# Performance work log

Hardware: AMD Instinct MI355X
Metric: run time of the kernel (lower is better)

## Reference

```python
import jax, jax.numpy as jnp
import numpy as np

N, E = 50000, 800000
NFEAT, NHID, NCLASS = 128, 64, 40
LN_EPS = 1e-5


def setup_inputs() -> dict:
    key = jax.random.key(0)
    ks = jax.random.split(key, 10)
    x = jax.random.normal(ks[0], (N, NFEAT), dtype=jnp.float32)
    edge_index = jax.random.randint(ks[1], (2, E), 0, N, dtype=jnp.int32)
    adj_vals = jax.random.uniform(ks[2], (E,), dtype=jnp.float32)
    s1 = 1.0 / NHID ** 0.5
    W1 = jax.random.uniform(ks[3], (NFEAT, NHID), minval=-s1, maxval=s1, dtype=jnp.float32)
    s2 = 1.0 / (2 * NHID) ** 0.5
    a1 = jax.random.uniform(ks[4], (2 * NHID, 1), minval=-s2, maxval=s2, dtype=jnp.float32)
    s3 = 1.0 / NCLASS ** 0.5
    W2 = jax.random.uniform(ks[5], (NHID, NCLASS), minval=-s3, maxval=s3, dtype=jnp.float32)
    # residual projection Linear(nfeat, nclass)
    sl = 1.0 / NFEAT ** 0.5
    res_w = jax.random.uniform(ks[6], (NCLASS, NFEAT), minval=-sl, maxval=sl, dtype=jnp.float32)
    res_b = jax.random.uniform(ks[7], (NCLASS,), minval=-sl, maxval=sl, dtype=jnp.float32)
    ln_g = jnp.ones((NCLASS,), dtype=jnp.float32)
    ln_b = jnp.zeros((NCLASS,), dtype=jnp.float32)
    return {"x": x, "edge_index": edge_index, "adj_vals": adj_vals,
            "W1": W1, "a1": a1, "W2": W2, "res_w": res_w, "res_b": res_b,
            "ln_g": ln_g, "ln_b": ln_b}


def reference(x, edge_index, adj_vals, W1, a1, W2, res_w, res_b, ln_g, ln_b):
    n = x.shape[0]
    row, col = edge_index[0], edge_index[1]
    h1 = x @ W1                                  # [N, nhid]
    # edge attention: cat([h1[row], h1[col]]) @ a1 == h1[row]@a_src + h1[col]@a_dst
    a_src, a_dst = a1[:NHID, 0], a1[NHID:, 0]
    scores = h1[row] @ a_src + h1[col] @ a_dst   # [E]
    scores = jax.nn.leaky_relu(scores, negative_slope=0.2)
    w = jax.nn.sigmoid(scores) * adj_vals        # [E] weighted adjacency values
    # sparse mm: out[row] += w * h[col]
    h1_out = jax.ops.segment_sum(w[:, None] * h1[col], row, num_segments=n)
    h1_out = jax.nn.relu(h1_out)
    h2 = h1_out @ W2                             # [N, nclass]
    h2_out = jax.ops.segment_sum(w[:, None] * h2[col], row, num_segments=n)
    h2_out = jax.nn.relu(h2_out)
    # residual projection + LayerNorm
    y = h2_out + (x @ res_w.T + res_b)
    mu = jnp.mean(y, axis=-1, keepdims=True)
    var = jnp.var(y, axis=-1, keepdims=True)
    y = (y - mu) * jax.lax.rsqrt(var + LN_EPS) * ln_g + ln_b
    return y
```

## Files before the change

kernel.cpp:

```cpp
#include <hip/hip_runtime.h>
#include <math.h>

#define N_NODES 50000
#define N_EDGES 800000
#define NFEAT 128
#define NHID 64
#define NCLASS 40
#define LN_EPS 1e-5f
#define BROWS 64
#define NBUCK ((N_NODES + BROWS - 1) / BROWS)
#define CHUNK 4096
#define NCHUNK ((N_EDGES + CHUNK - 1) / CHUNK)
#define NPB 16
#define H2ROWS 64
#define H2STRIDE 48

__device__ __forceinline__ int swz(int k) { return ((k >> 2) & 7) << 2; }

__device__ __forceinline__ unsigned packbf(float a, float b) {
  unsigned ua = __float_as_uint(a), ub = __float_as_uint(b);
  ua += 0x7fffu + ((ua >> 16) & 1u);
  ub += 0x7fffu + ((ub >> 16) & 1u);
  return (ua >> 16) | (ub & 0xffff0000u);
}
__device__ __forceinline__ unsigned bf16hi(float a) {
  unsigned u = __float_as_uint(a);
  u += 0x7fffu + ((u >> 16) & 1u);
  return u & 0xffff0000u;
}
__device__ __forceinline__ float lo16(unsigned v) { return __uint_as_float(v << 16); }
__device__ __forceinline__ float hi16(unsigned v) { return __uint_as_float(v & 0xffff0000u); }

__global__ __launch_bounds__(256) void k_h1mm(const float* __restrict__ x,
    const float* __restrict__ W1, const float* __restrict__ a1,
    unsigned* __restrict__ h1u, float* __restrict__ s_src, float* __restrict__ s_dst,
    int* __restrict__ bcnt) {
  __shared__ float xT[NFEAT * 64];
  __shared__ float W1s[NFEAT * NHID];
  int t = threadIdx.x;
  if (blockIdx.x == 0)
    for (int i = t; i < NBUCK; i += 256) bcnt[i] = 0;
  int R0 = blockIdx.x * 64;
  for (int i = t; i < NFEAT * NHID / 4; i += 256)
    ((float4*)W1s)[i] = ((const float4*)W1)[i];
#pragma unroll
  for (int it = 0; it < 8; ++it) {
    int i = t + it * 256;
    int r = i >> 5, kq = i & 31;
    int gr = R0 + r;
    float4 v = make_float4(0.f, 0.f, 0.f, 0.f);
    if (gr < N_NODES) v = *(const float4*)(x + (size_t)gr * NFEAT + kq * 4);
    int rw = r ^ ((kq & 7) << 2);
    xT[(kq * 4 + 0) * 64 + rw] = v.x;
    xT[(kq * 4 + 1) * 64 + rw] = v.y;
    xT[(kq * 4 + 2) * 64 + rw] = v.z;
    xT[(kq * 4 + 3) * 64 + rw] = v.w;
  }
  __syncthreads();
  int cg = t & 15, rg = t >> 4;
  int c0 = cg * 4, r0 = rg * 4;
  float acc[4][4] = {};
#pragma unroll 4
  for (int k = 0; k < NFEAT; ++k) {
    float4 xv = *(const float4*)&xT[k * 64 + (r0 ^ swz(k))];
    float4 wv = *(const float4*)&W1s[k * NHID + c0];
    float xr[4] = {xv.x, xv.y, xv.z, xv.w};
    float wr[4] = {wv.x, wv.y, wv.z, wv.w};
#pragma unroll
    for (int j = 0; j < 4; ++j)
#pragma unroll
      for (int c = 0; c < 4; ++c)
        acc[j][c] = fmaf(xr[j], wr[c], acc[j][c]);
  }
  float4 as = *(const float4*)(a1 + c0);
  float4 ad = *(const float4*)(a1 + NHID + c0);
  float asr[4] = {as.x, as.y, as.z, as.w};
  float adr[4] = {ad.x, ad.y, ad.z, ad.w};
  float ps[4], pd[4];
#pragma unroll
  for (int j = 0; j < 4; ++j) {
    int gr = R0 + r0 + j;
    if (gr < N_NODES) {
      uint2 pk;
      pk.x = packbf(acc[j][0], acc[j][1]);
      pk.y = packbf(acc[j][2], acc[j][3]);
      *(uint2*)&h1u[(size_t)gr * 32 + (c0 >> 1)] = pk;
    }
    float s = 0.f, d = 0.f;
#pragma unroll
    for (int c = 0; c < 4; ++c) {
      s = fmaf(acc[j][c], asr[c], s);
      d = fmaf(acc[j][c], adr[c], d);
    }
    ps[j] = s; pd[j] = d;
  }
#pragma unroll
  for (int j = 0; j < 4; ++j)
#pragma unroll
    for (int off = 1; off < 16; off <<= 1) {
      ps[j] += __shfl_xor(ps[j], off);
      pd[j] += __shfl_xor(pd[j], off);
    }
  if (cg == 0) {
#pragma unroll
    for (int j = 0; j < 4; ++j) {
      int gr = R0 + r0 + j;
      if (gr < N_NODES) { s_src[gr] = ps[j]; s_dst[gr] = pd[j]; }
    }
  }
}

__global__ __launch_bounds__(256) void k_resmm(const float* __restrict__ x,
    const float* __restrict__ res_w, const float* __restrict__ res_b,
    float* __restrict__ res, const int* __restrict__ ei, int* __restrict__ bcnt) {
  __shared__ float xT[NFEAT * 128];
  __shared__ float rwT[NFEAT * NCLASS];
  int t = threadIdx.x;
  int R0 = blockIdx.x * 128;
  for (int i = t; i < NCLASS * NFEAT; i += 256) {
    int c = i / NFEAT, k = i % NFEAT;
    rwT[k * NCLASS + c] = res_w[i];
  }
#pragma unroll
  for (int it = 0; it < 16; ++it) {
    int i = t + it * 256;
    int r = i >> 5, kq = i & 31;
    int gr = R0 + r;
    float4 v = make_float4(0.f, 0.f, 0.f, 0.f);
    if (gr < N_NODES) v = *(const float4*)(x + (size_t)gr * NFEAT + kq * 4);
    int rw = r ^ ((kq & 7) << 2);
    xT[(kq * 4 + 0) * 128 + rw] = v.x;
    xT[(kq * 4 + 1) * 128 + rw] = v.y;
    xT[(kq * 4 + 2) * 128 + rw] = v.z;
    xT[(kq * 4 + 3) * 128 + rw] = v.w;
  }
  __syncthreads();
  int cg = t & 7, rg = t >> 3;
  int c0 = cg * 5, r0 = rg * 4;
  float acc[4][5] = {};
#pragma unroll 4
  for (int k = 0; k < NFEAT; ++k) {
    float4 xv = *(const float4*)&xT[k * 128 + (r0 ^ swz(k))];
    float xr[4] = {xv.x, xv.y, xv.z, xv.w};
    float wr[5];
#pragma unroll
    for (int c = 0; c < 5; ++c) wr[c] = rwT[k * NCLASS + c0 + c];
#pragma unroll
    for (int j = 0; j < 4; ++j)
#pragma unroll
      for (int c = 0; c < 5; ++c)
        acc[j][c] = fmaf(xr[j], wr[c], acc[j][c]);
  }
  float bb[5];
#pragma unroll
  for (int c = 0; c < 5; ++c) bb[c] = res_b[c0 + c];
#pragma unroll
  for (int j = 0; j < 4; ++j) {
    int gr = R0 + r0 + j;
    if (gr < N_NODES) {
#pragma unroll
      for (int c = 0; c < 5; ++c)
        res[(size_t)gr * NCLASS + c0 + c] = acc[j][c] + bb[c];
    }
  }
  if (blockIdx.x < NCHUNK) {
    __syncthreads();
    int* cnt = (int*)xT;
    for (int i = t; i < NBUCK; i += 256) cnt[i] = 0;
    __syncthreads();
    int e0 = blockIdx.x * CHUNK;
    int ecnt = min(CHUNK, N_EDGES - e0);
    for (int i = t; i < ecnt; i += 256)
      atomicAdd(&cnt[ei[e0 + i] >> 6], 1);
    __syncthreads();
    for (int i = t; i < NBUCK; i += 256)
      if (cnt[i]) atomicAdd(&bcnt[i], cnt[i]);
  }
}

__global__ __launch_bounds__(256) void k_bscan(const int* __restrict__ bcnt,
    int* __restrict__ gptr, int* __restrict__ gfill) {
  __shared__ int psum[256];
  int t = threadIdx.x;
  int base = t * 4;
  int s[4];
#pragma unroll
  for (int j = 0; j < 4; ++j)
    s[j] = (base + j < NBUCK) ? bcnt[base + j] : 0;
  int local = s[0] + s[1] + s[2] + s[3];
  psum[t] = local;
  __syncthreads();
#pragma unroll
  for (int o = 1; o < 256; o <<= 1) {
    int v = (t >= o) ? psum[t - o] : 0;
    __syncthreads();
    psum[t] += v;
    __syncthreads();
  }
  int excl = psum[t] - local;
#pragma unroll
  for (int j = 0; j < 4; ++j) {
    if (base + j < NBUCK) gptr[base + j] = excl;
    excl += s[j];
  }
  if (t == 255) gptr[NBUCK] = psum[255];
  for (int i = t; i < NBUCK; i += 256) gfill[i] = 0;
}

__global__ __launch_bounds__(256) void k_bscatter(const int* __restrict__ ei,
    const float* __restrict__ adj, const int* __restrict__ gptr,
    int* __restrict__ gfill, uint2* __restrict__ edata) {
  __shared__ int cnt[NBUCK];
  __shared__ int off[NBUCK];
  __shared__ int gbase[NBUCK];
  __shared__ int po[NBUCK];
  __shared__ int psum[256];
  __shared__ uint2 stage[CHUNK];
  int t = threadIdx.x;
  int e0 = blockIdx.x * CHUNK;
  int ecnt = min(CHUNK, N_EDGES - e0);
  for (int i = t; i < NBUCK; i += 256) { cnt[i] = 0; po[i] = 0; }
  __syncthreads();
  for (int i = t; i < ecnt; i += 256)
    atomicAdd(&cnt[ei[e0 + i] >> 6], 1);
  __syncthreads();
  int base = t * 4;
  int s0 = (base < NBUCK) ? cnt[base] : 0;
  int s1 = (base + 1 < NBUCK) ? cnt[base + 1] : 0;
  int s2 = (base + 2 < NBUCK) ? cnt[base + 2] : 0;
  int s3 = (base + 3 < NBUCK) ? cnt[base + 3] : 0;
  int local = s0 + s1 + s2 + s3;
  psum[t] = local;
  __syncthreads();
#pragma unroll
  for (int o = 1; o < 256; o <<= 1) {
    int v = (t >= o) ? psum[t - o] : 0;
    __syncthreads();
    psum[t] += v;
    __syncthreads();
  }
  int excl = psum[t] - local;
  if (base < NBUCK) {
    off[base] = excl;
    if (s0 > 0) gbase[base] = gptr[base] + atomicAdd(&gfill[base], s0);
  }
  if (base + 1 < NBUCK) {
    off[base + 1] = excl + s0;
    if (s1 > 0) gbase[base + 1] = gptr[base + 1] + atomicAdd(&gfill[base + 1], s1);
  }
  if (base + 2 < NBUCK) {
    off[base + 2] = excl + s0 + s1;
    if (s2 > 0) gbase[base + 2] = gptr[base + 2] + atomicAdd(&gfill[base + 2], s2);
  }
  if (base + 3 < NBUCK) {
    off[base + 3] = excl + s0 + s1 + s2;
    if (s3 > 0) gbase[base + 3] = gptr[base + 3] + atomicAdd(&gfill[base + 3], s3);
  }
  __syncthreads();
  for (int i = t; i < ecnt; i += 256) {
    int e = e0 + i;
    int row = ei[e], col = ei[N_EDGES + e];
    int b = row >> 6;
    int pos = off[b] + atomicAdd(&po[b], 1);
    stage[pos] = make_uint2(((unsigned)b << 22) | ((unsigned)(row & 63) << 16) |
                            (unsigned)col, __float_as_uint(adj[e]));
  }
  __syncthreads();
  for (int i = t; i < ecnt; i += 256) {
    uint2 v = stage[i];
    int b = v.x >> 22;
    edata[(size_t)gbase[b] + (i - off[b])] = v;
  }
}

__global__ __launch_bounds__(256) void k_csr(const uint2* __restrict__ edata,
    const int* __restrict__ gptr, const float* __restrict__ s_src,
    const float* __restrict__ s_dst, int* __restrict__ row_ptr,
    unsigned* __restrict__ ecsr) {
  __shared__ int lcnt[BROWS];
  __shared__ int lexcl[BROWS];
  __shared__ int lfill[BROWS];
  __shared__ float ssrc[BROWS];
  int t = threadIdx.x;
  int b = blockIdx.x;
  int es = gptr[b], ee = gptr[b + 1];
  if (t < BROWS) {
    lcnt[t] = 0; lfill[t] = 0;
    int gn = b * BROWS + t;
    ssrc[t] = (gn < N_NODES) ? s_src[gn] : 0.f;
  }
  __syncthreads();
  for (int i = es + t; i < ee; i += 256)
    atomicAdd(&lcnt[(edata[i].x >> 16) & 63u], 1);
  __syncthreads();
  if (t < 64) {
    int v = lcnt[t];
    int sc = v;
#pragma unroll
    for (int o = 1; o < 64; o <<= 1) {
      int u = __shfl_up(sc, o);
      if (t >= o) sc += u;
    }
    lexcl[t] = sc - v;
    int gn = b * BROWS + t;
    if (gn < N_NODES) row_ptr[gn] = es + sc - v;
  }
  if (b == NBUCK - 1 && t == 0) row_ptr[N_NODES] = ee;
  __syncthreads();
  for (int i = es + t; i < ee; i += 256) {
    uint2 v = edata[i];
    int rl = (v.x >> 16) & 63;
    int col = v.x & 0xffffu;
    float sc = ssrc[rl] + s_dst[col];
    sc = (sc > 0.f) ? sc : 0.2f * sc;
    float wv = __uint_as_float(v.y) / (1.f + __expf(-sc));
    int pos = es + lexcl[rl] + atomicAdd(&lfill[rl], 1);
    ecsr[pos] = bf16hi(wv) | (unsigned)col;
  }
}

__global__ __launch_bounds__(256) void k_agg1(const unsigned* __restrict__ h1u,
    const unsigned* __restrict__ edata, const int* __restrict__ row_ptr,
    unsigned* __restrict__ h1o) {
  __shared__ int rps[NPB + 1];
  __shared__ float accs[NPB][NHID];
  int t = threadIdx.x;
  int n0 = blockIdx.x * NPB;
  if (t <= NPB) rps[t] = row_ptr[min(n0 + t, N_NODES)];
  for (int i = t; i < NPB * NHID / 4; i += 256)
    ((float4*)&accs[0][0])[i] = make_float4(0.f, 0.f, 0.f, 0.f);
  __syncthreads();
  int e0 = rps[0], e1 = rps[NPB];
  int span = e1 - e0;
  int gid = t >> 5, s = t & 31;
  int chunk = (span + 7) >> 3;
  int es = e0 + gid * chunk;
  int ee = min(es + chunk, e1);
  if (es < ee) {
    int lo = 0, hi = NPB - 1;
    while (lo < hi) { int mid = (lo + hi) >> 1; if (rps[mid + 1] <= es) lo = mid + 1; else hi = mid; }
    int r = lo, nxt = rps[r + 1];
    float acc0 = 0.f, acc1 = 0.f;
    int e = es;
    while (e < ee) {
      int m = ee - e; if (m > 8) m = 8;
      unsigned ue = (s < m) ? edata[e + s] : 0u;
      unsigned u[8], v[8];
#pragma unroll
      for (int i = 0; i < 8; ++i) u[i] = __shfl(ue, i, 32);
#pragma unroll
      for (int i = 0; i < 8; ++i) if (i < m) v[i] = h1u[(size_t)(u[i] & 0xffffu) * 32 + s];
#pragma unroll
      for (int i = 0; i < 8; ++i) if (i < m) {
        while (e + i >= nxt) {
          atomicAdd(&accs[r][2 * s], acc0);
          atomicAdd(&accs[r][2 * s + 1], acc1);
          acc0 = acc1 = 0.f; ++r; nxt = rps[r + 1];
        }
        float wv = hi16(u[i]);
        acc0 = fmaf(wv, lo16(v[i]), acc0);
        acc1 = fmaf(wv, hi16(v[i]), acc1);
      }
      e += m;
    }
    atomicAdd(&accs[r][2 * s], acc0);
    atomicAdd(&accs[r][2 * s + 1], acc1);
  }
  __syncthreads();
  for (int i = t; i < NPB * 32; i += 256) {
    int n = i >> 5, c = i & 31;
    int gn = n0 + n;
    if (gn < N_NODES)
      h1o[(size_t)gn * 32 + c] =
          packbf(fmaxf(accs[n][2 * c], 0.f), fmaxf(accs[n][2 * c + 1], 0.f));
  }
}

__global__ __launch_bounds__(256) void k_h2mm(const unsigned* __restrict__ h1o,
    const float* __restrict__ W2, unsigned short* __restrict__ h2s) {
  __shared__ unsigned xs[H2ROWS * 32];
  __shared__ float W2s[NHID * NCLASS];
  int t = threadIdx.x;
  int R0 = blockIdx.x * H2ROWS;
  for (int i = t; i < NHID * NCLASS; i += 256) W2s[i] = W2[i];
  for (int i = t; i < H2ROWS * 32; i += 256) {
    int r = i >> 5, ku = i & 31;
    int gr = R0 + r;
    unsigned v = (gr < N_NODES) ? h1o[(size_t)gr * 32 + ku] : 0u;
    xs[r * 32 + (ku ^ (r & 31))] = v;
  }
  __syncthreads();
  int q = t & 31, cg = t >> 5;
  int c0 = cg * 5;
  float acc[2][5] = {};
#pragma unroll 8
  for (int ku = 0; ku < 32; ++ku) {
    unsigned ua = xs[q * 32 + (ku ^ q)];
    unsigned ub = xs[(q + 32) * 32 + (ku ^ q)];
    float a0 = lo16(ua), a1 = hi16(ua);
    float b0 = lo16(ub), b1 = hi16(ub);
#pragma unroll
    for (int c = 0; c < 5; ++c) {
      float w0 = W2s[(2 * ku) * NCLASS + c0 + c];
      float w1 = W2s[(2 * ku + 1) * NCLASS + c0 + c];
      acc[0][c] = fmaf(a0, w0, acc[0][c]);
      acc[0][c] = fmaf(a1, w1, acc[0][c]);
      acc[1][c] = fmaf(b0, w0, acc[1][c]);
      acc[1][c] = fmaf(b1, w1, acc[1][c]);
    }
  }
#pragma unroll
  for (int j = 0; j < 2; ++j) {
    int gr = R0 + q + j * 32;
    if (gr < N_NODES) {
#pragma unroll
      for (int c = 0; c < 5; ++c)
        h2s[(size_t)gr * H2STRIDE + c0 + c] = (unsigned short)(bf16hi(acc[j][c]) >> 16);
    }
  }
}

__global__ __launch_bounds__(256) void k_agg2(const unsigned short* __restrict__ h2s,
    const unsigned* __restrict__ edata, const int* __restrict__ row_ptr,
    const float* __restrict__ res, const float* __restrict__ ln_g,
    const float* __restrict__ ln_b, float* __restrict__ out) {
  __shared__ int rps[NPB + 1];
  __shared__ float accs[NPB][NCLASS];
  int t = threadIdx.x;
  int n0 = blockIdx.x * NPB;
  if (t <= NPB) rps[t] = row_ptr[min(n0 + t, N_NODES)];
  for (int i = t; i < NPB * NCLASS; i += 256) ((float*)accs)[i] = 0.f;
  __syncthreads();
  int e0 = rps[0], e1 = rps[NPB];
  int span = e1 - e0;
  int gid = t >> 5, s = t & 31;
  int chunk = (span + 7) >> 3;
  int es = e0 + gid * chunk;
  int ee = min(es + chunk, e1);
  bool act = (s < 20);
  if (es < ee) {
    int lo = 0, hi = NPB - 1;
    while (lo < hi) { int mid = (lo + hi) >> 1; if (rps[mid + 1] <= es) lo = mid + 1; else hi = mid; }
    int r = lo, nxt = rps[r + 1];
    float acc0 = 0.f, acc1 = 0.f;
    int e = es;
    while (e < ee) {
      int m = ee - e; if (m > 8) m = 8;
      unsigned ue = (s < m) ? edata[e + s] : 0u;
      unsigned u[8], v[8];
#pragma unroll
      for (int i = 0; i < 8; ++i) u[i] = __shfl(ue, i, 32);
#pragma unroll
      for (int i = 0; i < 8; ++i) {
        v[i] = 0u;
        if (i < m && act)
          v[i] = *(const unsigned*)(h2s + (size_t)(u[i] & 0xffffu) * H2STRIDE + 2 * s);
      }
#pragma unroll
      for (int i = 0; i < 8; ++i) if (i < m) {
        while (e + i >= nxt) {
          if (act) {
            atomicAdd(&accs[r][2 * s], acc0);
            atomicAdd(&accs[r][2 * s + 1], acc1);
          }
          acc0 = acc1 = 0.f; ++r; nxt = rps[r + 1];
        }
        float wv = hi16(u[i]);
        acc0 = fmaf(wv, lo16(v[i]), acc0);
        acc1 = fmaf(wv, hi16(v[i]), acc1);
      }
      e += m;
    }
    if (act) {
      atomicAdd(&accs[r][2 * s], acc0);
      atomicAdd(&accs[r][2 * s + 1], acc1);
    }
  }
  __syncthreads();
  int wave = t >> 6, lane = t & 63;
  for (int k = 0; k < NPB / 4; ++k) {
    int n = wave * (NPB / 4) + k;
    int gn = n0 + n;
    if (gn >= N_NODES) break;
    float y = 0.f;
    if (lane < NCLASS)
      y = fmaxf(accs[n][lane], 0.f) + res[(size_t)gn * NCLASS + lane];
    float s1 = y, s2 = y * y;
#pragma unroll
    for (int off = 1; off < 64; off <<= 1) {
      s1 += __shfl_xor(s1, off);
      s2 += __shfl_xor(s2, off);
    }
    float mu = s1 / (float)NCLASS;
    float var = s2 / (float)NCLASS - mu * mu;
    float inv = rsqrtf(var + LN_EPS);
    if (lane < NCLASS)
      out[(size_t)gn * NCLASS + lane] = (y - mu) * inv * ln_g[lane] + ln_b[lane];
  }
}

extern "C" void kernel_launch(void* const* d_in, const int* in_sizes, int n_in,
                              void* d_out, int out_size, void* d_ws, size_t ws_size,
                              hipStream_t stream) {
  const float* x     = (const float*)d_in[0];
  const int*   ei    = (const int*)  d_in[1];
  const float* adj   = (const float*)d_in[2];
  const float* W1    = (const float*)d_in[3];
  const float* a1    = (const float*)d_in[4];
  const float* W2    = (const float*)d_in[5];
  const float* res_w = (const float*)d_in[6];
  const float* res_b = (const float*)d_in[7];
  const float* ln_g  = (const float*)d_in[8];
  const float* ln_b  = (const float*)d_in[9];
  float* out = (float*)d_out;

  char* ws = (char*)d_ws;
  size_t off = 0;
  auto alloc = [&](size_t bytes) -> void* {
    void* p = (void*)(ws + off);
    off += (bytes + 255) & ~(size_t)255;
    return p;
  };

  unsigned*       h1u     = (unsigned*)alloc((size_t)N_NODES * 32 * 4);
  float*          s_src   = (float*)alloc((size_t)N_NODES * 4);
  float*          s_dst   = (float*)alloc((size_t)N_NODES * 4);
  int*            bcnt    = (int*)alloc((size_t)NBUCK * 4);
  int*            gptr    = (int*)alloc((size_t)(NBUCK + 1) * 4);
  int*            gfill   = (int*)alloc((size_t)NBUCK * 4);
  int*            row_ptr = (int*)alloc((size_t)(N_NODES + 1) * 4);
  uint2*          edata   = (uint2*)alloc((size_t)N_EDGES * 8);
  unsigned*       ecsr    = (unsigned*)alloc((size_t)N_EDGES * 4);
  unsigned*       h1o     = (unsigned*)alloc((size_t)N_NODES * 32 * 4);
  unsigned short* h2s     = (unsigned short*)alloc((size_t)N_NODES * H2STRIDE * 2);
  float*          res     = (float*)alloc((size_t)N_NODES * NCLASS * 4);
  (void)ws_size; (void)in_sizes; (void)n_in; (void)out_size;

  const int NBLK_H1  = (N_NODES + 63) / 64;
  const int NBLK_RES = (N_NODES + 127) / 128;
  const int NBLK_H2  = (N_NODES + H2ROWS - 1) / H2ROWS;
  const int NBLK_AGG = (N_NODES + NPB - 1) / NPB;

  k_h1mm<<<NBLK_H1, 256, 0, stream>>>(x, W1, a1, h1u, s_src, s_dst, bcnt);
  k_resmm<<<NBLK_RES, 256, 0, stream>>>(x, res_w, res_b, res, ei, bcnt);
  k_bscan<<<1, 256, 0, stream>>>(bcnt, gptr, gfill);
  k_bscatter<<<NCHUNK, 256, 0, stream>>>(ei, adj, gptr, gfill, edata);
  k_csr<<<NBUCK, 256, 0, stream>>>(edata, gptr, s_src, s_dst, row_ptr, ecsr);
  k_agg1<<<NBLK_AGG, 256, 0, stream>>>(h1u, ecsr, row_ptr, h1o);
  k_h2mm<<<NBLK_H2, 256, 0, stream>>>(h1o, W2, h2s);
  k_agg2<<<NBLK_AGG, 256, 0, stream>>>(h2s, ecsr, row_ptr, res, ln_g, ln_b, out);
}
```

Measured before the change: 190.2 us.

## Fuse second-layer matmul into first aggregation and halve scatter chunk size

The h1_out @ W2 projection moves into the epilogue of the first aggregation kernel. Each block loads W2 into shared memory, applies ReLU to its fp32 accumulators and writes the bf16 h2 rows directly, which removes the h1o intermediate round trip and one kernel launch. It also keeps h1_out in fp32 instead of rounding it to bf16 before the matmul. The bucket-scatter kernel now uses 2048-edge chunks, giving more blocks and less staging shared memory. The cost is an extra 10 KB of shared memory and a W2 reload in every aggregation block, plus a naive per-thread 64-length dot product that may lower occupancy.

```diff
diff --git a/kernel.cpp b/kernel.cpp
--- a/kernel.cpp
+++ b/kernel.cpp
@@ -11,8 +11,9 @@
 #define NBUCK ((N_NODES + BROWS - 1) / BROWS)
 #define CHUNK 4096
 #define NCHUNK ((N_EDGES + CHUNK - 1) / CHUNK)
+#define SCHUNK 2048
+#define SNCHUNK ((N_EDGES + SCHUNK - 1) / SCHUNK)
 #define NPB 16
-#define H2ROWS 64
 #define H2STRIDE 48
 
 __device__ __forceinline__ int swz(int k) { return ((k >> 2) & 7) << 2; }
@@ -215,10 +216,10 @@
   __shared__ int gbase[NBUCK];
   __shared__ int po[NBUCK];
   __shared__ int psum[256];
-  __shared__ uint2 stage[CHUNK];
-  int t = threadIdx.x;
-  int e0 = blockIdx.x * CHUNK;
-  int ecnt = min(CHUNK, N_EDGES - e0);
+  __shared__ uint2 stage[SCHUNK];
+  int t = threadIdx.x;
+  int e0 = blockIdx.x * SCHUNK;
+  int ecnt = min(SCHUNK, N_EDGES - e0);
   for (int i = t; i < NBUCK; i += 256) { cnt[i] = 0; po[i] = 0; }
   __syncthreads();
   for (int i = t; i < ecnt; i += 256)
@@ -321,12 +322,14 @@
 
 __global__ __launch_bounds__(256) void k_agg1(const unsigned* __restrict__ h1u,
     const unsigned* __restrict__ edata, const int* __restrict__ row_ptr,
-    unsigned* __restrict__ h1o) {
+    const float* __restrict__ W2, unsigned short* __restrict__ h2s) {
   __shared__ int rps[NPB + 1];
   __shared__ float accs[NPB][NHID];
+  __shared__ float W2s[NHID * NCLASS];
   int t = threadIdx.x;
   int n0 = blockIdx.x * NPB;
   if (t <= NPB) rps[t] = row_ptr[min(n0 + t, N_NODES)];
+  for (int i = t; i < NHID * NCLASS; i += 256) W2s[i] = W2[i];
   for (int i = t; i < NPB * NHID / 4; i += 256)
     ((float4*)&accs[0][0])[i] = make_float4(0.f, 0.f, 0.f, 0.f);
   __syncthreads();
@@ -367,55 +370,18 @@
     atomicAdd(&accs[r][2 * s + 1], acc1);
   }
   __syncthreads();
-  for (int i = t; i < NPB * 32; i += 256) {
-    int n = i >> 5, c = i & 31;
+  for (int i = t; i < NPB * NHID; i += 256)
+    ((float*)accs)[i] = fmaxf(((float*)accs)[i], 0.f);
+  __syncthreads();
+  for (int idx = t; idx < NPB * NCLASS; idx += 256) {
+    int n = idx / NCLASS, c = idx % NCLASS;
     int gn = n0 + n;
-    if (gn < N_NODES)
-      h1o[(size_t)gn * 32 + c] =
-          packbf(fmaxf(accs[n][2 * c], 0.f), fmaxf(accs[n][2 * c + 1], 0.f));
-  }
-}
-
-__global__ __launch_bounds__(256) void k_h2mm(const unsigned* __restrict__ h1o,
-    const float* __restrict__ W2, unsigned short* __restrict__ h2s) {
-  __shared__ unsigned xs[H2ROWS * 32];
-  __shared__ float W2s[NHID * NCLASS];
-  int t = threadIdx.x;
-  int R0 = blockIdx.x * H2ROWS;
-  for (int i = t; i < NHID * NCLASS; i += 256) W2s[i] = W2[i];
-  for (int i = t; i < H2ROWS * 32; i += 256) {
-    int r = i >> 5, ku = i & 31;
-    int gr = R0 + r;
-    unsigned v = (gr < N_NODES) ? h1o[(size_t)gr * 32 + ku] : 0u;
-    xs[r * 32 + (ku ^ (r & 31))] = v;
-  }
-  __syncthreads();
-  int q = t & 31, cg = t >> 5;
-  int c0 = cg * 5;
-  float acc[2][5] = {};
+    if (gn < N_NODES) {
+      float sum = 0.f;
 #pragma unroll 8
-  for (int ku = 0; ku < 32; ++ku) {
-    unsigned ua = xs[q * 32 + (ku ^ q)];
-    unsigned ub = xs[(q + 32) * 32 + (ku ^ q)];
-    float a0 = lo16(ua), a1 = hi16(ua);
-    float b0 = lo16(ub), b1 = hi16(ub);
-#pragma unroll
-    for (int c = 0; c < 5; ++c) {
-      float w0 = W2s[(2 * ku) * NCLASS + c0 + c];
-      float w1 = W2s[(2 * ku + 1) * NCLASS + c0 + c];
-      acc[0][c] = fmaf(a0, w0, acc[0][c]);
-      acc[0][c] = fmaf(a1, w1, acc[0][c]);
-      acc[1][c] = fmaf(b0, w0, acc[1][c]);
-      acc[1][c] = fmaf(b1, w1, acc[1][c]);
-    }
-  }
-#pragma unroll
-  for (int j = 0; j < 2; ++j) {
-    int gr = R0 + q + j * 32;
-    if (gr < N_NODES) {
-#pragma unroll
-      for (int c = 0; c < 5; ++c)
-        h2s[(size_t)gr * H2STRIDE + c0 + c] = (unsigned short)(bf16hi(acc[j][c]) >> 16);
+      for (int j = 0; j < NHID; ++j)
+        sum = fmaf(accs[n][j], W2s[j * NCLASS + c], sum);
+      h2s[(size_t)gn * H2STRIDE + c] = (unsigned short)(bf16hi(sum) >> 16);
     }
   }
 }
@@ -531,22 +497,19 @@
   int*            row_ptr = (int*)alloc((size_t)(N_NODES + 1) * 4);
   uint2*          edata   = (uint2*)alloc((size_t)N_EDGES * 8);
   unsigned*       ecsr    = (unsigned*)alloc((size_t)N_EDGES * 4);
-  unsigned*       h1o     = (unsigned*)alloc((size_t)N_NODES * 32 * 4);
   unsigned short* h2s     = (unsigned short*)alloc((size_t)N_NODES * H2STRIDE * 2);
   float*          res     = (float*)alloc((size_t)N_NODES * NCLASS * 4);
   (void)ws_size; (void)in_sizes; (void)n_in; (void)out_size;
 
   const int NBLK_H1  = (N_NODES + 63) / 64;
   const int NBLK_RES = (N_NODES + 127) / 128;
-  const int NBLK_H2  = (N_NODES + H2ROWS - 1) / H2ROWS;
   const int NBLK_AGG = (N_NODES + NPB - 1) / NPB;
 
   k_h1mm<<<NBLK_H1, 256, 0, stream>>>(x, W1, a1, h1u, s_src, s_dst, bcnt);
   k_resmm<<<NBLK_RES, 256, 0, stream>>>(x, res_w, res_b, res, ei, bcnt);
   k_bscan<<<1, 256, 0, stream>>>(bcnt, gptr, gfill);
-  k_bscatter<<<NCHUNK, 256, 0, stream>>>(ei, adj, gptr, gfill, edata);
+  k_bscatter<<<SNCHUNK, 256, 0, stream>>>(ei, adj, gptr, gfill, edata);
   k_csr<<<NBUCK, 256, 0, stream>>>(edata, gptr, s_src, s_dst, row_ptr, ecsr);
-  k_agg1<<<NBLK_AGG, 256, 0, stream>>>(h1u, ecsr, row_ptr, h1o);
-  k_h2mm<<<NBLK_H2, 256, 0, stream>>>(h1o, W2, h2s);
+  k_agg1<<<NBLK_AGG, 256, 0, stream>>>(h1u, ecsr, row_ptr, W2, h2s);
   k_agg2<<<NBLK_AGG, 256, 0, stream>>>(h2s, ecsr, row_ptr, res, ln_g, ln_b, out);
 }
```

New measurement: 205.6 us. +8.1%, slower.
